# Optimization experiments

Hardware: AMD Instinct MI355X
Metric: run time of the kernel (lower is better)

The kernel has to match this reference:

```python
import jax, jax.numpy as jnp
import numpy as np
import math

B, L, D = 4, 2048, 128
DEGREE = 2
EPS = 1e-12  # F.normalize eps

# upper-triangular index pairs (i <= j), matching torch.triu_indices(D, D)
_TRIU_I, _TRIU_J = np.triu_indices(D)
TRIU_I = jnp.asarray(_TRIU_I)
TRIU_J = jnp.asarray(_TRIU_J)


def setup_inputs() -> dict:
    key = jax.random.key(0)
    k1, _ = jax.random.split(key)
    x = jax.random.normal(k1, (B, L, D), dtype=jnp.float32)
    degree_scales = jnp.ones((DEGREE,), dtype=jnp.float32) / math.sqrt(DEGREE)
    return {"x": x, "degree_scales": degree_scales}


def reference(x, degree_scales):
    # F.normalize(x, dim=-1): x / max(||x||_2, eps)
    norm = jnp.linalg.norm(x, axis=-1, keepdims=True)
    x_norm = x / jnp.maximum(norm, EPS)
    # degree-1 features (unscaled, matching the torch code)
    feats1 = x_norm
    # degree-2 features: only the needed upper-triangular products, no D^2 materialization
    deg2 = x_norm[..., TRIU_I] * x_norm[..., TRIU_J]  # (B, L, D*(D+1)/2)
    deg2 = deg2 * degree_scales[1]
    return jnp.concatenate([feats1, deg2], axis=-1)  # (B, L, D + D*(D+1)/2)
```

## Files before the change

kernel.cpp:

```cpp
#include <hip/hip_runtime.h>


#define DD 128
#define ROW_OUT (DD + DD * (DD + 1) / 2)
#define NCHUNK (ROW_OUT / 4)

__global__ __launch_bounds__(256) void poly_kernel(
    const float* __restrict__ x, const float* __restrict__ scales,
    float* __restrict__ out) {
  __shared__ float s_x[DD];
  __shared__ float s_c1;
  __shared__ float s_c2;

  const int row = blockIdx.x;
  const int tid = threadIdx.x;
  const float* xr = x + (size_t)row * DD;

  float partial = 0.0f;
  if (tid < 32) {
    float4 xv = ((const float4*)xr)[tid];
    ((float4*)s_x)[tid] = xv;
    partial = xv.x * xv.x + xv.y * xv.y + xv.z * xv.z + xv.w * xv.w;
  }
  if (tid < 64) {
#pragma unroll
    for (int off = 16; off >= 1; off >>= 1)
      partial += __shfl_down(partial, off, 64);
    if (tid == 0) {
      float nrm = sqrtf(partial);
      float inv = 1.0f / fmaxf(nrm, 1e-12f);
      s_c1 = inv;
      s_c2 = inv * inv * scales[1];
    }
  }
  __syncthreads();

  const float c1 = s_c1;
  const float c2 = s_c2;
  float* orow = out + (size_t)row * ROW_OUT;

  for (int p4 = tid; p4 < NCHUNK; p4 += 256) {
    const int p = p4 * 4;
    float4 v;
    if (p < DD) {
      float4 xv = ((const float4*)s_x)[p4];
      v = make_float4(xv.x * c1, xv.y * c1, xv.z * c1, xv.w * c1);
    } else {
      int k = p - DD;
      float r = sqrtf((float)(257 * 257 - 8 * k));
      int i = (int)((257.0f - r) * 0.5f);
      int off = (i * (257 - i)) >> 1;
      if (off > k) {
        --i;
        off = (i * (257 - i)) >> 1;
      } else {
        int off2 = ((i + 1) * (256 - i)) >> 1;
        if (off2 <= k) {
          ++i;
          off = off2;
        }
      }
      int j = i + (k - off);
      float xi = s_x[i] * c2;
      float vv[4];
#pragma unroll
      for (int e = 0; e < 4; ++e) {
        if (j >= DD) {
          ++i;
          j = i;
          xi = s_x[i] * c2;
        }
        vv[e] = xi * s_x[j];
        ++j;
      }
      v = make_float4(vv[0], vv[1], vv[2], vv[3]);
    }
    ((float4*)orow)[p4] = v;
  }
}

extern "C" void kernel_launch(void* const* d_in, const int* in_sizes, int n_in,
                              void* d_out, int out_size, void* d_ws,
                              size_t ws_size, hipStream_t stream) {
  const float* x = (const float*)d_in[0];
  const float* scales = (const float*)d_in[1];
  float* out = (float*)d_out;
  const int n_rows = in_sizes[0] / DD;
  poly_kernel<<<n_rows, 256, 0, stream>>>(x, scales, out);
}
```

Baseline: 280.9 us.

## Stage full output row in shared memory, then stream it out as float4

The kernel now builds the whole output row (normalized features plus upper-triangular products) in a shared-memory image. Each wavefront writes one triangle row at a time with simple contiguous indexing, then all threads copy the image to global memory with coalesced float4 stores. This removes the per-chunk sqrt-based triangle index inversion and its branching. In exchange it uses about 33 KB of LDS per block, which limits occupancy, and adds a second barrier plus a shared-memory round trip.

```diff
diff --git a/kernel.cpp b/kernel.cpp
--- a/kernel.cpp
+++ b/kernel.cpp
@@ -8,75 +8,41 @@
 __global__ __launch_bounds__(256) void poly_kernel(
     const float* __restrict__ x, const float* __restrict__ scales,
     float* __restrict__ out) {
-  __shared__ float s_x[DD];
-  __shared__ float s_c1;
-  __shared__ float s_c2;
+  __shared__ float s_img[ROW_OUT];
 
   const int row = blockIdx.x;
   const int tid = threadIdx.x;
-  const float* xr = x + (size_t)row * DD;
+  const float s1 = scales[1];
 
-  float partial = 0.0f;
-  if (tid < 32) {
-    float4 xv = ((const float4*)xr)[tid];
-    ((float4*)s_x)[tid] = xv;
-    partial = xv.x * xv.x + xv.y * xv.y + xv.z * xv.z + xv.w * xv.w;
-  }
   if (tid < 64) {
+    float4 xv = make_float4(0.f, 0.f, 0.f, 0.f);
+    if (tid < 32) xv = ((const float4*)(x + (size_t)row * DD))[tid];
+    float partial = xv.x * xv.x + xv.y * xv.y + xv.z * xv.z + xv.w * xv.w;
 #pragma unroll
     for (int off = 16; off >= 1; off >>= 1)
       partial += __shfl_down(partial, off, 64);
-    if (tid == 0) {
-      float nrm = sqrtf(partial);
-      float inv = 1.0f / fmaxf(nrm, 1e-12f);
-      s_c1 = inv;
-      s_c2 = inv * inv * scales[1];
-    }
+    float total = __shfl(partial, 0, 64);
+    float inv = 1.0f / fmaxf(sqrtf(total), 1e-12f);
+    if (tid < 32)
+      ((float4*)s_img)[tid] =
+          make_float4(xv.x * inv, xv.y * inv, xv.z * inv, xv.w * inv);
   }
   __syncthreads();
 
-  const float c1 = s_c1;
-  const float c2 = s_c2;
+  const int w = tid >> 6;
+  const int lane = tid & 63;
+  for (int i = w; i < DD; i += 4) {
+    const float xi = s_img[i] * s1;
+    const int len = DD - i;
+    const int base = DD + ((i * (2 * DD + 1 - i)) >> 1);
+    for (int l = lane; l < len; l += 64)
+      s_img[base + l] = xi * s_img[i + l];
+  }
+  __syncthreads();
+
   float* orow = out + (size_t)row * ROW_OUT;
-
-  for (int p4 = tid; p4 < NCHUNK; p4 += 256) {
-    const int p = p4 * 4;
-    float4 v;
-    if (p < DD) {
-      float4 xv = ((const float4*)s_x)[p4];
-      v = make_float4(xv.x * c1, xv.y * c1, xv.z * c1, xv.w * c1);
-    } else {
-      int k = p - DD;
-      float r = sqrtf((float)(257 * 257 - 8 * k));
-      int i = (int)((257.0f - r) * 0.5f);
-      int off = (i * (257 - i)) >> 1;
-      if (off > k) {
-        --i;
-        off = (i * (257 - i)) >> 1;
-      } else {
-        int off2 = ((i + 1) * (256 - i)) >> 1;
-        if (off2 <= k) {
-          ++i;
-          off = off2;
-        }
-      }
-      int j = i + (k - off);
-      float xi = s_x[i] * c2;
-      float vv[4];
-#pragma unroll
-      for (int e = 0; e < 4; ++e) {
-        if (j >= DD) {
-          ++i;
-          j = i;
-          xi = s_x[i] * c2;
-        }
-        vv[e] = xi * s_x[j];
-        ++j;
-      }
-      v = make_float4(vv[0], vv[1], vv[2], vv[3]);
-    }
-    ((float4*)orow)[p4] = v;
-  }
+  for (int p4 = tid; p4 < NCHUNK; p4 += 256)
+    ((float4*)orow)[p4] = ((const float4*)s_img)[p4];
 }
 
 extern "C" void kernel_launch(void* const* d_in, const int* in_sizes, int n_in,
```

Measured after the change: 294.1 us. 4.7% more time.
